# Optimization experiments

Measured on AMD Instinct MI355X. Metric: run time of the kernel, lower is better.

## Reference

```python
import jax, jax.numpy as jnp
import numpy as np

N = 100_000   # nodes
E = 1_600_000  # edges (avg degree 16)
D_IN, D_HID, D_OUT = 128, 128, 64


def setup_inputs() -> dict:
    key = jax.random.key(0)
    k = jax.random.split(key, 6)
    x = jax.random.normal(k[0], (N, D_IN), dtype=jnp.float32)
    edge_index = jax.random.randint(k[1], (2, E), 0, N, dtype=jnp.int32)
    W1 = jax.random.normal(k[2], (D_IN, D_HID), dtype=jnp.float32) / np.sqrt(D_IN)
    b1 = jnp.zeros((D_HID,), dtype=jnp.float32)
    W2 = jax.random.normal(k[3], (D_HID, D_OUT), dtype=jnp.float32) / np.sqrt(D_HID)
    b2 = jnp.zeros((D_OUT,), dtype=jnp.float32)
    return {"x": x, "edge_index": edge_index, "W1": W1, "b1": b1, "W2": W2, "b2": b2}


def reference(x, edge_index, W1, b1, W2, b2):
    # GCNConv (PyG defaults): add self-loops, symmetric deg^-1/2 normalization,
    # linear transform then sum-aggregate over neighbors, then bias.
    loop = jnp.arange(N, dtype=edge_index.dtype)
    src = jnp.concatenate([edge_index[0], loop])  # [E+N]
    dst = jnp.concatenate([edge_index[1], loop])  # [E+N]

    deg = jax.ops.segment_sum(jnp.ones(src.shape, jnp.float32), dst, num_segments=N)
    inv_sqrt_deg = jnp.where(deg > 0, jax.lax.rsqrt(jnp.maximum(deg, 1.0)), 0.0)
    coef = (inv_sqrt_deg[src] * inv_sqrt_deg[dst])[:, None]  # [E+N, 1]

    def gcn_conv(h, W, b):
        h = h @ W                                   # [N, d_out]
        msg = h[src] * coef                          # gather + scale, [E+N, d_out]
        return jax.ops.segment_sum(msg, dst, num_segments=N) + b

    h = jax.nn.relu(gcn_conv(x, W1, b1))
    # dropout is identity in eval mode
    return gcn_conv(h, W2, b2)
```

## Files before the change

kernel.cpp:

```cpp
#include <hip/hip_runtime.h>

#define NN 100000
#define NE 1600000
#define DI 128
#define DH 128
#define DO 64
#define NBK 98
#define SLOT 18432
#define PAD 16
#define EPB 8192
#define NSB ((NE + EPB - 1) / EPB)

typedef unsigned int uint;
typedef unsigned short ushort;
typedef unsigned char uchar;
typedef __bf16 bf16x8 __attribute__((ext_vector_type(8)));
typedef float f32x4 __attribute__((ext_vector_type(4)));

__device__ __forceinline__ float bf_lo(uint u) { return __uint_as_float(u << 16); }
__device__ __forceinline__ float bf_hi(uint u) { return __uint_as_float(u & 0xffff0000u); }
__device__ __forceinline__ ushort f2bf(float f) {
    uint u = __float_as_uint(f);
    uint r = u + 0x7fffu + ((u >> 16) & 1u);
    return (ushort)(r >> 16);
}

__global__ void k_binit(int* __restrict__ bcur) {
    int t = threadIdx.x;
    if (t < NBK) bcur[t * PAD] = t * SLOT;
}

__global__ __launch_bounds__(512) void k_bscatter(const int* __restrict__ src,
                                                  const int* __restrict__ dst,
                                                  int* __restrict__ bcur,
                                                  uint* __restrict__ ebuf) {
    __shared__ uint stage[EPB];
    __shared__ uchar bktid[EPB];
    __shared__ int lcnt[NBK];
    __shared__ int loff[NBK];
    __shared__ int gbase[NBK];
    int t = threadIdx.x;
    int e0 = blockIdx.x * EPB;
    int n = min(EPB, NE - e0);
    for (int i = t; i < NBK; i += 512) lcnt[i] = 0;
    __syncthreads();
    for (int i = t; i < n; i += 512)
        atomicAdd(&lcnt[dst[e0 + i] >> 10], 1);
    __syncthreads();
    if (t == 0) {
        int r = 0;
        for (int i = 0; i < NBK; ++i) { loff[i] = r; r += lcnt[i]; }
    }
    __syncthreads();
    if (t < NBK) {
        gbase[t] = atomicAdd(&bcur[t * PAD], lcnt[t]);
        lcnt[t] = loff[t];
    }
    __syncthreads();
    for (int i = t; i < n; i += 512) {
        int d = dst[e0 + i];
        int s = src[e0 + i];
        int b = d >> 10;
        int p = atomicAdd(&lcnt[b], 1);
        stage[p] = ((uint)s << 10) | (uint)(d & 1023);
        bktid[p] = (uchar)b;
    }
    __syncthreads();
    for (int j = t; j < n; j += 512) {
        int b = bktid[j];
        ebuf[gbase[b] + (j - loff[b])] = stage[j];
    }
}

__global__ __launch_bounds__(1024) void k_bfill(const uint* __restrict__ ebuf,
                                                const int* __restrict__ bcur,
                                                uint2* __restrict__ offdeg,
                                                float* __restrict__ inv,
                                                int* __restrict__ csr_src) {
    __shared__ int cnt[1024];
    __shared__ int s[1024];
    __shared__ int cur[1024];
    int b = blockIdx.x, t = threadIdx.x;
    int ebeg = b * SLOT;
    int eend = bcur[b * PAD];
    cnt[t] = 0;
    __syncthreads();
    for (int e = ebeg + t; e < eend; e += 1024)
        atomicAdd(&cnt[ebuf[e] & 1023], 1);
    __syncthreads();
    int v = cnt[t];
    s[t] = v;
    __syncthreads();
    for (int d = 1; d < 1024; d <<= 1) {
        int a = (t >= d) ? s[t - d] : 0;
        __syncthreads();
        s[t] += a;
        __syncthreads();
    }
    int beg = ebeg + s[t] - v;
    int node = b * 1024 + t;
    if (node < NN) {
        offdeg[node] = make_uint2((uint)beg, (uint)v);
        inv[node] = rsqrtf((float)v + 1.0f);
    }
    cur[t] = beg;
    __syncthreads();
    for (int e = ebeg + t; e < eend; e += 1024) {
        uint ed = ebuf[e];
        int p = atomicAdd(&cur[ed & 1023], 1);
        csr_src[p] = (int)(ed >> 10);
    }
}

__global__ void k_wt(const float* __restrict__ W, ushort* __restrict__ Wt, int K, int N) {
    int t = blockIdx.x * blockDim.x + threadIdx.x;
    if (t < K * N) {
        int c = t / K, k = t % K;
        Wt[t] = f2bf(W[k * N + c]);
    }
}

template <int N, bool ABF16>
__global__ __launch_bounds__(256) void k_gemm_mfma(const void* __restrict__ Ap,
                                                   const ushort* __restrict__ Wt,
                                                   const float* __restrict__ inv,
                                                   ushort* __restrict__ out) {
    int wid = threadIdx.x >> 6;
    int lane = threadIdx.x & 63;
    int r0 = (blockIdx.x * 4 + wid) * 32;
    if (r0 >= NN) return;
    int rlo = lane & 15, khi = lane >> 4;

    constexpr int CT = N / 16;
    f32x4 acc[2][CT] = {};

#pragma unroll
    for (int ks = 0; ks < 4; ++ks) {
        bf16x8 bf[CT];
#pragma unroll
        for (int ct = 0; ct < CT; ++ct)
            bf[ct] = *(const bf16x8*)(Wt + (ct * 16 + rlo) * 128 + ks * 32 + khi * 8);
#pragma unroll
        for (int rt = 0; rt < 2; ++rt) {
            int row = r0 + rt * 16 + rlo;
            bf16x8 af;
            if (ABF16) {
                af = *(const bf16x8*)((const ushort*)Ap + (size_t)row * 128 + ks * 32 + khi * 8);
            } else {
                const float* pa = (const float*)Ap + (size_t)row * 128 + ks * 32 + khi * 8;
                float4 f0 = *(const float4*)pa;
                float4 f1 = *(const float4*)(pa + 4);
                af[0] = (__bf16)f0.x; af[1] = (__bf16)f0.y;
                af[2] = (__bf16)f0.z; af[3] = (__bf16)f0.w;
                af[4] = (__bf16)f1.x; af[5] = (__bf16)f1.y;
                af[6] = (__bf16)f1.z; af[7] = (__bf16)f1.w;
            }
#pragma unroll
            for (int ct = 0; ct < CT; ++ct)
                acc[rt][ct] = __builtin_amdgcn_mfma_f32_16x16x32_bf16(af, bf[ct], acc[rt][ct], 0, 0, 0);
        }
    }
#pragma unroll
    for (int rt = 0; rt < 2; ++rt) {
        int rowb = r0 + rt * 16 + 4 * khi;
#pragma unroll
        for (int b = 0; b < 4; ++b) {
            float sc = inv[rowb + b];
#pragma unroll
            for (int ct = 0; ct < CT; ++ct)
                out[(size_t)(rowb + b) * N + ct * 16 + rlo] = f2bf(acc[rt][ct][b] * sc);
        }
    }
}

template <bool RELU>
__global__ void k_agg128(const uint2* __restrict__ offdeg, const int* __restrict__ csr,
                         const ushort* __restrict__ tab, const float* __restrict__ inv,
                         const float* __restrict__ bias, ushort* __restrict__ outb) {
    int wid = threadIdx.x >> 6, lane = threadIdx.x & 63;
    int node = blockIdx.x * (blockDim.x >> 6) + wid;
    if (node >= NN) return;
    uint2 od = offdeg[node];
    int beg = (int)od.x, end = beg + (int)od.y;
    const uint* t32 = (const uint*)tab;
    float a0 = 0.f, a1 = 0.f;
    int e = beg;
    for (; e + 3 < end; e += 4) {
        int s0 = csr[e], s1 = csr[e + 1], s2 = csr[e + 2], s3 = csr[e + 3];
        uint u0 = t32[(size_t)s0 * 64 + lane];
        uint u1 = t32[(size_t)s1 * 64 + lane];
        uint u2 = t32[(size_t)s2 * 64 + lane];
        uint u3 = t32[(size_t)s3 * 64 + lane];
        a0 += bf_lo(u0); a1 += bf_hi(u0);
        a0 += bf_lo(u1); a1 += bf_hi(u1);
        a0 += bf_lo(u2); a1 += bf_hi(u2);
        a0 += bf_lo(u3); a1 += bf_hi(u3);
    }
    for (; e < end; ++e) {
        int s = csr[e];
        uint u = t32[(size_t)s * 64 + lane];
        a0 += bf_lo(u); a1 += bf_hi(u);
    }
    float invd = inv[node];
    uint us = t32[(size_t)node * 64 + lane];
    float2 b = *(const float2*)(bias + lane * 2);
    float r0 = fmaf(invd, a0 + bf_lo(us), b.x);
    float r1 = fmaf(invd, a1 + bf_hi(us), b.y);
    if (RELU) { r0 = fmaxf(r0, 0.f); r1 = fmaxf(r1, 0.f); }
    uint packed = (uint)f2bf(r0) | ((uint)f2bf(r1) << 16);
    *(uint*)(outb + (size_t)node * 128 + lane * 2) = packed;
}

__global__ void k_agg64(const uint2* __restrict__ offdeg, const int* __restrict__ csr,
                        const ushort* __restrict__ tab, const float* __restrict__ inv,
                        const float* __restrict__ bias, float* __restrict__ out) {
    int wid = threadIdx.x >> 6, lane = threadIdx.x & 63;
    int node = blockIdx.x * (blockDim.x >> 6) + wid;
    if (node >= NN) return;
    uint2 od = offdeg[node];
    int beg = (int)od.x, end = beg + (int)od.y;
    float a0 = 0.f;
    int e = beg;
    for (; e + 3 < end; e += 4) {
        int s0 = csr[e], s1 = csr[e + 1], s2 = csr[e + 2], s3 = csr[e + 3];
        float h0 = __uint_as_float((uint)tab[(size_t)s0 * 64 + lane] << 16);
        float h1 = __uint_as_float((uint)tab[(size_t)s1 * 64 + lane] << 16);
        float h2 = __uint_as_float((uint)tab[(size_t)s2 * 64 + lane] << 16);
        float h3 = __uint_as_float((uint)tab[(size_t)s3 * 64 + lane] << 16);
        a0 += h0; a0 += h1; a0 += h2; a0 += h3;
    }
    for (; e < end; ++e) {
        int s = csr[e];
        a0 += __uint_as_float((uint)tab[(size_t)s * 64 + lane] << 16);
    }
    float invd = inv[node];
    float hs = __uint_as_float((uint)tab[(size_t)node * 64 + lane] << 16);
    out[(size_t)node * 64 + lane] = fmaf(invd, a0 + hs, bias[lane]);
}

extern "C" void kernel_launch(void* const* d_in, const int* in_sizes, int n_in,
                              void* d_out, int out_size, void* d_ws, size_t ws_size,
                              hipStream_t stream) {
    const float* x  = (const float*)d_in[0];
    const int* ei   = (const int*)d_in[1];
    const int* src  = ei;
    const int* dst  = ei + NE;
    const float* W1 = (const float*)d_in[2];
    const float* b1 = (const float*)d_in[3];
    const float* W2 = (const float*)d_in[4];
    const float* b2 = (const float*)d_in[5];
    float* out = (float*)d_out;

    uint2*  offdeg  = (uint2*)d_ws;
    float*  inv     = (float*)(offdeg + NN);
    int*    bcur    = (int*)(inv + 100004);
    int*    csr_src = bcur + NBK * PAD;
    ushort* w1t     = (ushort*)(csr_src + NBK * SLOT);
    ushort* w2t     = w1t + 128 * 128;
    ushort* h       = w2t + 64 * 128;
    ushort* hagg    = h + (size_t)NN * DH;
    ushort* h2      = hagg + (size_t)NN * DH;
    uint*   ebuf    = (uint*)h2;

    k_binit<<<1, 128, 0, stream>>>(bcur);
    k_bscatter<<<NSB, 512, 0, stream>>>(src, dst, bcur, ebuf);
    k_bfill<<<NBK, 1024, 0, stream>>>(ebuf, bcur, offdeg, inv, csr_src);

    k_wt<<<64, 256, 0, stream>>>(W1, w1t, 128, 128);
    k_wt<<<32, 256, 0, stream>>>(W2, w2t, 128, 64);

    k_gemm_mfma<DH, false><<<(NN + 127) / 128, 256, 0, stream>>>(x, w1t, inv, h);
    k_agg128<true><<<NN / 4, 256, 0, stream>>>(offdeg, csr_src, h, inv, b1, hagg);

    k_gemm_mfma<DO, true><<<(NN + 127) / 128, 256, 0, stream>>>(hagg, w2t, inv, h2);
    k_agg64<<<NN / 4, 256, 0, stream>>>(offdeg, csr_src, h2, inv, b2, out);
}
```

Measured before the change: 251.0 us.

## Use finer 256-node buckets for CSR build and fuse weight prep kernels

Shrinks CSR-construction buckets from 1024 to 256 nodes, giving 391 buckets. The fill kernel then launches 391 blocks of 256 threads instead of 98 blocks of 1024, which spreads work across more CUs. The per-block bucket offsets in the scatter kernel now come from a parallel scan instead of a serial loop on thread 0. The bucket-cursor init and both weight transposes are merged into one launch. The costs are more global atomic cursors per scatter block, a wider shared bucket-id array, and a larger scan.

```diff
diff --git a/kernel.cpp b/kernel.cpp
--- a/kernel.cpp
+++ b/kernel.cpp
@@ -5,15 +5,14 @@
 #define DI 128
 #define DH 128
 #define DO 64
-#define NBK 98
-#define SLOT 18432
+#define NBK 391
+#define SLOT 5120
 #define PAD 16
 #define EPB 8192
 #define NSB ((NE + EPB - 1) / EPB)
 
 typedef unsigned int uint;
 typedef unsigned short ushort;
-typedef unsigned char uchar;
 typedef __bf16 bf16x8 __attribute__((ext_vector_type(8)));
 typedef float f32x4 __attribute__((ext_vector_type(4)));
 
@@ -25,9 +24,19 @@
     return (ushort)(r >> 16);
 }
 
-__global__ void k_binit(int* __restrict__ bcur) {
-    int t = threadIdx.x;
+__global__ void k_prep(const float* __restrict__ W1, const float* __restrict__ W2,
+                       ushort* __restrict__ w1t, ushort* __restrict__ w2t,
+                       int* __restrict__ bcur) {
+    int t = blockIdx.x * 256 + threadIdx.x;
     if (t < NBK) bcur[t * PAD] = t * SLOT;
+    if (t < 128 * 128) {
+        int c = t >> 7, k = t & 127;
+        w1t[t] = f2bf(W1[k * 128 + c]);
+    } else if (t < 128 * 128 + 64 * 128) {
+        int u = t - 128 * 128;
+        int c = u >> 7, k = u & 127;
+        w2t[u] = f2bf(W2[k * 64 + c]);
+    }
 }
 
 __global__ __launch_bounds__(512) void k_bscatter(const int* __restrict__ src,
@@ -35,35 +44,41 @@
                                                   int* __restrict__ bcur,
                                                   uint* __restrict__ ebuf) {
     __shared__ uint stage[EPB];
-    __shared__ uchar bktid[EPB];
+    __shared__ ushort bktid[EPB];
     __shared__ int lcnt[NBK];
     __shared__ int loff[NBK];
     __shared__ int gbase[NBK];
+    __shared__ int s[512];
     int t = threadIdx.x;
     int e0 = blockIdx.x * EPB;
     int n = min(EPB, NE - e0);
     for (int i = t; i < NBK; i += 512) lcnt[i] = 0;
     __syncthreads();
     for (int i = t; i < n; i += 512)
-        atomicAdd(&lcnt[dst[e0 + i] >> 10], 1);
-    __syncthreads();
-    if (t == 0) {
-        int r = 0;
-        for (int i = 0; i < NBK; ++i) { loff[i] = r; r += lcnt[i]; }
-    }
-    __syncthreads();
+        atomicAdd(&lcnt[dst[e0 + i] >> 8], 1);
+    __syncthreads();
+    int myc = (t < NBK) ? lcnt[t] : 0;
+    s[t] = myc;
+    __syncthreads();
+    for (int d = 1; d < 512; d <<= 1) {
+        int a = (t >= d) ? s[t - d] : 0;
+        __syncthreads();
+        s[t] += a;
+        __syncthreads();
+    }
     if (t < NBK) {
-        gbase[t] = atomicAdd(&bcur[t * PAD], lcnt[t]);
-        lcnt[t] = loff[t];
+        loff[t] = s[t] - myc;
+        gbase[t] = atomicAdd(&bcur[t * PAD], myc);
+        lcnt[t] = s[t] - myc;
     }
     __syncthreads();
     for (int i = t; i < n; i += 512) {
         int d = dst[e0 + i];
-        int s = src[e0 + i];
-        int b = d >> 10;
+        int sv = src[e0 + i];
+        int b = d >> 8;
         int p = atomicAdd(&lcnt[b], 1);
-        stage[p] = ((uint)s << 10) | (uint)(d & 1023);
-        bktid[p] = (uchar)b;
+        stage[p] = ((uint)sv << 8) | (uint)(d & 255);
+        bktid[p] = (ushort)b;
     }
     __syncthreads();
     for (int j = t; j < n; j += 512) {
@@ -72,51 +87,43 @@
     }
 }
 
-__global__ __launch_bounds__(1024) void k_bfill(const uint* __restrict__ ebuf,
-                                                const int* __restrict__ bcur,
-                                                uint2* __restrict__ offdeg,
-                                                float* __restrict__ inv,
-                                                int* __restrict__ csr_src) {
-    __shared__ int cnt[1024];
-    __shared__ int s[1024];
-    __shared__ int cur[1024];
+__global__ __launch_bounds__(256) void k_bfill(const uint* __restrict__ ebuf,
+                                               const int* __restrict__ bcur,
+                                               uint2* __restrict__ offdeg,
+                                               float* __restrict__ inv,
+                                               int* __restrict__ csr_src) {
+    __shared__ int cnt[256];
+    __shared__ int s[256];
+    __shared__ int cur[256];
     int b = blockIdx.x, t = threadIdx.x;
     int ebeg = b * SLOT;
     int eend = bcur[b * PAD];
     cnt[t] = 0;
     __syncthreads();
-    for (int e = ebeg + t; e < eend; e += 1024)
-        atomicAdd(&cnt[ebuf[e] & 1023], 1);
+    for (int e = ebeg + t; e < eend; e += 256)
+        atomicAdd(&cnt[ebuf[e] & 255], 1);
     __syncthreads();
     int v = cnt[t];
     s[t] = v;
     __syncthreads();
-    for (int d = 1; d < 1024; d <<= 1) {
+    for (int d = 1; d < 256; d <<= 1) {
         int a = (t >= d) ? s[t - d] : 0;
         __syncthreads();
         s[t] += a;
         __syncthreads();
     }
     int beg = ebeg + s[t] - v;
-    int node = b * 1024 + t;
+    int node = b * 256 + t;
     if (node < NN) {
         offdeg[node] = make_uint2((uint)beg, (uint)v);
         inv[node] = rsqrtf((float)v + 1.0f);
     }
     cur[t] = beg;
     __syncthreads();
-    for (int e = ebeg + t; e < eend; e += 1024) {
+    for (int e = ebeg + t; e < eend; e += 256) {
         uint ed = ebuf[e];
-        int p = atomicAdd(&cur[ed & 1023], 1);
-        csr_src[p] = (int)(ed >> 10);
-    }
-}
-
-__global__ void k_wt(const float* __restrict__ W, ushort* __restrict__ Wt, int K, int N) {
-    int t = blockIdx.x * blockDim.x + threadIdx.x;
-    if (t < K * N) {
-        int c = t / K, k = t % K;
-        Wt[t] = f2bf(W[k * N + c]);
+        int p = atomicAdd(&cur[ed & 255], 1);
+        csr_src[p] = (int)(ed >> 8);
     }
 }
 
@@ -262,12 +269,9 @@
     ushort* h2      = hagg + (size_t)NN * DH;
     uint*   ebuf    = (uint*)h2;
 
-    k_binit<<<1, 128, 0, stream>>>(bcur);
+    k_prep<<<96, 256, 0, stream>>>(W1, W2, w1t, w2t, bcur);
     k_bscatter<<<NSB, 512, 0, stream>>>(src, dst, bcur, ebuf);
-    k_bfill<<<NBK, 1024, 0, stream>>>(ebuf, bcur, offdeg, inv, csr_src);
-
-    k_wt<<<64, 256, 0, stream>>>(W1, w1t, 128, 128);
-    k_wt<<<32, 256, 0, stream>>>(W2, w2t, 128, 64);
+    k_bfill<<<NBK, 256, 0, stream>>>(ebuf, bcur, offdeg, inv, csr_src);
 
     k_gemm_mfma<DH, false><<<(NN + 127) / 128, 256, 0, stream>>>(x, w1t, inv, h);
     k_agg128<true><<<NN / 4, 256, 0, stream>>>(offdeg, csr_src, h, inv, b1, hagg);
```

Result: faster. 244.3 us (-2.7%).
